# Performance work log

Hardware: AMD Instinct MI355X
Metric: run time of the kernel (lower is better)

Reference implementation:

```python
import jax, jax.numpy as jnp
import numpy as np

N_HEAD = 12

def setup_inputs() -> dict:
    key = jax.random.key(0)
    k1, k2, k3 = jax.random.split(key, 3)
    nx = 768
    B, S = 2, 2048
    return {
        "hidden_states": jax.random.normal(k1, (B, S, nx), dtype=jnp.float32),
        "w_attn": jax.random.normal(k2, (nx, 3 * nx), dtype=jnp.float32) * 0.02,
        "b_attn": jnp.zeros((3 * nx,), dtype=jnp.float32),
        "w_proj": jax.random.normal(k3, (nx, nx), dtype=jnp.float32) * 0.02,
        "b_proj": jnp.zeros((nx,), dtype=jnp.float32),
    }

def reference(hidden_states, w_attn, b_attn, w_proj, b_proj):
    B, S, nx = hidden_states.shape
    d_head = nx // N_HEAD
    qkv = hidden_states @ w_attn + b_attn  # [B,S,3nx]
    q, k, v = jnp.split(qkv, 3, axis=-1)
    # split heads -> [B,H,S,d]
    def split(x):
        return x.reshape(B, S, N_HEAD, d_head).transpose(0, 2, 1, 3)
    q, k, v = split(q), split(k), split(v)
    # scale=True: divide by sqrt(d_head) (v.size(-1))
    w = jnp.einsum("bhsd,bhtd->bhst", q, k) / jnp.sqrt(jnp.float32(d_head))
    w = jax.nn.softmax(w, axis=-1)
    a = jnp.einsum("bhst,bhtd->bhsd", w, v)  # [B,H,S,d]
    a = a.transpose(0, 2, 1, 3).reshape(B, S, nx)  # merge heads
    return a @ w_proj + b_proj
```

## Files before the change

kernel.cpp:

```cpp
#include <hip/hip_runtime.h>

#define NHEAD 12
#define DHEAD 64
#define SEQ   2048
#define NB    2
#define NX    768
#define MTOK  (NB * SEQ)

typedef __attribute__((ext_vector_type(8))) short short8;
typedef __attribute__((ext_vector_type(4))) short short4v;
typedef __attribute__((ext_vector_type(4))) float f32x4;

__device__ __forceinline__ unsigned short f2bf(float x) {
    union { float f; unsigned u; } v; v.f = x;
    unsigned r = v.u + 0x7fffu + ((v.u >> 16) & 1u);
    return (unsigned short)(r >> 16);
}

#define MFMA32(a, b, c) __builtin_amdgcn_mfma_f32_16x16x32_bf16(a, b, c, 0, 0, 0)
#define MFMA16(a, b, c) __builtin_amdgcn_mfma_f32_16x16x16bf16_1k(a, b, c, 0, 0, 0)

__global__ __launch_bounds__(256)
void cvt_all(const float* __restrict__ hs,
             const float* __restrict__ wa, const float* __restrict__ wp,
             unsigned short* __restrict__ Abf,
             unsigned short* __restrict__ WtA, unsigned short* __restrict__ WtP)
{
    __shared__ float tile[32][33];
    const int bid = blockIdx.x;
    const int t = threadIdx.x;

    if (bid < 3072) {
        int i = bid * 256 + t;
        if (i >= 786432) return;
        float4 v = ((const float4*)hs)[i];
        ushort4 o;
        o.x = f2bf(v.x); o.y = f2bf(v.y); o.z = f2bf(v.z); o.w = f2bf(v.w);
        ((ushort4*)Abf)[i] = o;
        return;
    }

    const float* W; unsigned short* T; int K, N, bx, by;
    if (bid < 4800) {
        int b2 = bid - 3072;
        bx = b2 % 72; by = b2 / 72;
        W = wa; T = WtA; K = NX; N = 3 * NX;
    } else {
        int b2 = bid - 4800;
        bx = b2 % 24; by = b2 / 24;
        W = wp; T = WtP; K = NX; N = NX;
    }
    const int r = t >> 5, c = t & 31;
    const int k0 = by * 32, n0 = bx * 32;
#pragma unroll
    for (int i = 0; i < 4; i++)
        tile[r + i * 8][c] = W[(size_t)(k0 + r + i * 8) * N + n0 + c];
    __syncthreads();
#pragma unroll
    for (int i = 0; i < 4; i++) {
        int n = r + i * 8;
        T[(size_t)(n0 + n) * K + k0 + c] = f2bf(tile[c][n]);
    }
}

template<int MODE>
__global__ __launch_bounds__(256, 3)
void gemm_bf(const unsigned short* __restrict__ A,
             const unsigned short* __restrict__ Bt,
             const float* __restrict__ bias,
             float* __restrict__ fo,
             unsigned short* __restrict__ qb, unsigned short* __restrict__ kb2,
             unsigned short* __restrict__ vtb,
             int M, int N, int K)
{
    __shared__ __align__(16) unsigned char sm[2][16384];
    const int t = threadIdx.x;
    const int w = t >> 6, lane = t & 63;
    const int lo16 = lane & 15, quad = lane >> 4;
    const int ib = blockIdx.y * 128, jb = blockIdx.x * 128;

    f32x4 acc[4][4];
#pragma unroll
    for (int mt = 0; mt < 4; mt++)
#pragma unroll
        for (int nt = 0; nt < 4; nt++) acc[mt][nt] = (f32x4){0.f, 0.f, 0.f, 0.f};

    const int srow = lane >> 2;
    const int sj   = lane & 3;

    auto stage = [&](int buf, int k0) {
#pragma unroll
        for (int i = 0; i < 4; i++) {
            const int u   = i * 4 + w;
            const int p   = u >> 3;
            const int row = (u & 7) * 16 + srow;
            const int sc  = sj ^ (row & 3);
            const unsigned short* g = (p == 0)
                ? (A  + (size_t)(ib + row) * K + k0 + sc * 8)
                : (Bt + (size_t)(jb + row) * K + k0 + sc * 8);
            void* lp = &sm[buf][p * 8192 + (u & 7) * 1024];
            __builtin_amdgcn_global_load_lds(
                (const __attribute__((address_space(1))) unsigned int*)g,
                (__attribute__((address_space(3))) unsigned int*)lp, 16, 0, 0);
        }
    };

    const int mrow = (w >> 1) * 64;
    const int nrow = (w & 1) * 64;

    stage(0, 0);
    const int NIT = K / 32;
    for (int kt = 0; kt < NIT; kt++) {
        const int buf = kt & 1;
        __syncthreads();
        if (kt + 1 < NIT) stage(buf ^ 1, (kt + 1) * 32);

        short8 af[4], bf[4];
#pragma unroll
        for (int mt = 0; mt < 4; mt++) {
            const int row = mrow + mt * 16 + lo16;
            af[mt] = *(const short8*)&sm[buf][row * 64 + ((quad ^ (row & 3)) * 16)];
        }
#pragma unroll
        for (int nt = 0; nt < 4; nt++) {
            const int row = nrow + nt * 16 + lo16;
            bf[nt] = *(const short8*)&sm[buf][8192 + row * 64 + ((quad ^ (row & 3)) * 16)];
        }
#pragma unroll
        for (int mt = 0; mt < 4; mt++)
#pragma unroll
            for (int nt = 0; nt < 4; nt++)
                acc[mt][nt] = MFMA32(af[mt], bf[nt], acc[mt][nt]);
    }

    if constexpr (MODE == 0) {
        const int which = jb / NX;
#pragma unroll
        for (int nt = 0; nt < 4; nt++) {
            const int j  = jb + nrow + nt * 16 + lo16;
            const int cc = j - which * NX;
            const int hh = cc >> 6, dd = cc & 63;
            const float bj = bias[j];
#pragma unroll
            for (int mt = 0; mt < 4; mt++) {
                const int m0 = ib + mrow + mt * 16 + quad * 4;
                const int bb = m0 >> 11;
                const int s0 = m0 & 2047;
                const size_t hb = (size_t)(bb * NHEAD + hh);
                if (which == 2) {
                    ushort4 pv;
                    pv.x = f2bf(acc[mt][nt][0] + bj);
                    pv.y = f2bf(acc[mt][nt][1] + bj);
                    pv.z = f2bf(acc[mt][nt][2] + bj);
                    pv.w = f2bf(acc[mt][nt][3] + bj);
                    *(ushort4*)(vtb + (hb * DHEAD + dd) * SEQ + s0) = pv;
                } else {
                    unsigned short* dst = (which == 0) ? qb : kb2;
                    const float sc = (which == 0) ? 0.125f : 1.0f;
#pragma unroll
                    for (int r = 0; r < 4; r++)
                        dst[(hb * SEQ + s0 + r) * DHEAD + dd] =
                            f2bf((acc[mt][nt][r] + bj) * sc);
                }
            }
        }
    } else {
#pragma unroll
        for (int nt = 0; nt < 4; nt++) {
            const int j  = jb + nrow + nt * 16 + lo16;
            const float bj = bias[j];
#pragma unroll
            for (int mt = 0; mt < 4; mt++) {
                const int m0 = ib + mrow + mt * 16 + quad * 4;
#pragma unroll
                for (int r = 0; r < 4; r++)
                    fo[(size_t)(m0 + r) * N + j] = acc[mt][nt][r] + bj;
            }
        }
    }
}

__global__ __launch_bounds__(256, 3)
void attn_bf(const unsigned short* __restrict__ qb, const unsigned short* __restrict__ kb,
             const unsigned short* __restrict__ vtb, unsigned short* __restrict__ ab)
{
    __shared__ __align__(16) unsigned char sm[2][16384];
    const int t = threadIdx.x;
    const int w = t >> 6, lane = t & 63;
    const int lo16 = lane & 15, quad = lane >> 4;

    const int id = blockIdx.x;
    const int xcd = id & 7, slot = id >> 3;
    const int bh = xcd * 3 + slot % 3;
    const int q0 = (slot / 3) * 64;
    const int b = bh / NHEAD, h = bh % NHEAD;

    const unsigned short* Qb = qb  + (size_t)bh * SEQ * DHEAD;
    const unsigned short* Kb = kb  + (size_t)bh * SEQ * DHEAD;
    const unsigned short* Vb = vtb + (size_t)bh * DHEAD * SEQ;

    short8 qf[2];
    {
        const size_t qo = (size_t)(q0 + w * 16 + lo16) * DHEAD + quad * 8;
        qf[0] = *(const short8*)(Qb + qo);
        qf[1] = *(const short8*)(Qb + qo + 32);
    }

    const int srow = lane >> 3;
    const int sj   = lane & 7;
    auto stage = [&](int buf, int k0) {
#pragma unroll
        for (int i = 0; i < 4; i++) {
            const int u   = i * 4 + w;
            const int p   = u >> 3;
            const int row = (u & 7) * 8 + srow;
            const int sc  = sj ^ (row & 7);
            const unsigned short* g = (p == 0)
                ? (Kb + (size_t)(k0 + row) * DHEAD + sc * 8)
                : (Vb + (size_t)row * SEQ + k0 + sc * 8);
            void* lp = &sm[buf][p * 8192 + (u & 7) * 1024];
            __builtin_amdgcn_global_load_lds(
                (const __attribute__((address_space(1))) unsigned int*)g,
                (__attribute__((address_space(3))) unsigned int*)lp, 16, 0, 0);
        }
    };

    f32x4 oacc[4];
#pragma unroll
    for (int dt = 0; dt < 4; dt++) oacc[dt] = (f32x4){0.f, 0.f, 0.f, 0.f};
    float lsum = 0.f;

    stage(0, 0);
    for (int kt = 0; kt < SEQ / 64; kt++) {
        const int buf = kt & 1;
        __syncthreads();
        if (kt + 1 < SEQ / 64) stage(buf ^ 1, (kt + 1) * 64);

        f32x4 s[4];
#pragma unroll
        for (int rt = 0; rt < 4; rt++) {
            const int row = rt * 16 + lo16;
            const int rs = row & 7;
            short8 kf0 = *(const short8*)&sm[buf][row * 128 + ((quad ^ rs) * 16)];
            short8 kf1 = *(const short8*)&sm[buf][row * 128 + (((4 + quad) ^ rs) * 16)];
            f32x4 a = (f32x4){0.f, 0.f, 0.f, 0.f};
            a = MFMA32(kf0, qf[0], a);
            a = MFMA32(kf1, qf[1], a);
            s[rt] = a;
        }

        short4v pf[4];
#pragma unroll
        for (int rt = 0; rt < 4; rt++) {
            float p0 = __expf(s[rt][0]), p1 = __expf(s[rt][1]);
            float p2 = __expf(s[rt][2]), p3 = __expf(s[rt][3]);
            lsum += (p0 + p1) + (p2 + p3);
            short4v pv;
            pv[0] = (short)f2bf(p0); pv[1] = (short)f2bf(p1);
            pv[2] = (short)f2bf(p2); pv[3] = (short)f2bf(p3);
            pf[rt] = pv;
        }

#pragma unroll
        for (int dt = 0; dt < 4; dt++) {
            const int row = dt * 16 + lo16;
            const int rs = row & 7;
            f32x4 a = oacc[dt];
#pragma unroll
            for (int rt = 0; rt < 4; rt++) {
                const int ch = (2 * rt + (quad >> 1)) ^ rs;
                short4v vf = *(const short4v*)&sm[buf][8192 + row * 128 + ch * 16 + (quad & 1) * 8];
                a = MFMA16(vf, pf[rt], a);
            }
            oacc[dt] = a;
        }
    }

    lsum += __shfl_xor(lsum, 16);
    lsum += __shfl_xor(lsum, 32);
    const float inv = 1.0f / lsum;

    unsigned short* dst = ab + (size_t)(b * SEQ + q0 + w * 16 + lo16) * NX + h * DHEAD;
#pragma unroll
    for (int dt = 0; dt < 4; dt++) {
        ushort4 pv;
        pv.x = f2bf(oacc[dt][0] * inv);
        pv.y = f2bf(oacc[dt][1] * inv);
        pv.z = f2bf(oacc[dt][2] * inv);
        pv.w = f2bf(oacc[dt][3] * inv);
        *(ushort4*)(dst + dt * 16 + quad * 4) = pv;
    }
}

extern "C" void kernel_launch(void* const* d_in, const int* in_sizes, int n_in,
                              void* d_out, int out_size, void* d_ws, size_t ws_size,
                              hipStream_t stream)
{
    const float* hs     = (const float*)d_in[0];
    const float* w_attn = (const float*)d_in[1];
    const float* b_attn = (const float*)d_in[2];
    const float* w_proj = (const float*)d_in[3];
    const float* b_proj = (const float*)d_in[4];
    float* out = (float*)d_out;

    unsigned short* wsu = (unsigned short*)d_ws;
    unsigned short* Abf  = wsu;
    unsigned short* WtA  = Abf  + 3145728;
    unsigned short* WtP  = WtA  + 1769472;
    unsigned short* qbuf = WtP  + 589824;
    unsigned short* kbuf = qbuf + 3145728;
    unsigned short* vtbf = kbuf + 3145728;
    unsigned short* abf  = vtbf + 3145728;

    cvt_all<<<5376, 256, 0, stream>>>(hs, w_attn, w_proj, Abf, WtA, WtP);

    gemm_bf<0><<<dim3(18, 32), 256, 0, stream>>>(
        Abf, WtA, b_attn, nullptr, qbuf, kbuf, vtbf, MTOK, 3 * NX, NX);

    attn_bf<<<768, 256, 0, stream>>>(qbuf, kbuf, vtbf, abf);

    gemm_bf<1><<<dim3(6, 32), 256, 0, stream>>>(
        abf, WtP, b_proj, out, nullptr, nullptr, nullptr, MTOK, NX, NX);
}
```

Measured before the change: 162.7 us.

## Split QKV GEMM into transposed Q/K and V launches, widen attention query tiles

The QKV GEMM is split into two launches. Q/K are computed with swapped operands so each lane writes contiguous ushort4 along the head dimension, and V keeps the transposed layout. The output projection is likewise swapped so it writes float4 rows. The attention kernel moves to 128 threads with two query tiles per wave, so each staged K/V tile feeds twice the MFMA work. Q is prescaled by log2(e)/sqrt(d) so exp2 can be used, and bf16 packing uses a byte-permute truncation instead of round-to-nearest, which costs a little precision and raises register pressure per wave.

```diff
diff --git a/kernel.cpp b/kernel.cpp
--- a/kernel.cpp
+++ b/kernel.cpp
@@ -19,6 +19,8 @@
 
 #define MFMA32(a, b, c) __builtin_amdgcn_mfma_f32_16x16x32_bf16(a, b, c, 0, 0, 0)
 #define MFMA16(a, b, c) __builtin_amdgcn_mfma_f32_16x16x16bf16_1k(a, b, c, 0, 0, 0)
+
+#define QSCALE 0.1803368801111204f
 
 __global__ __launch_bounds__(256)
 void cvt_all(const float* __restrict__ hs,
@@ -134,12 +136,10 @@
     }
 
     if constexpr (MODE == 0) {
-        const int which = jb / NX;
 #pragma unroll
         for (int nt = 0; nt < 4; nt++) {
             const int j  = jb + nrow + nt * 16 + lo16;
-            const int cc = j - which * NX;
-            const int hh = cc >> 6, dd = cc & 63;
+            const int hh = j >> 6, dd = j & 63;
             const float bj = bias[j];
 #pragma unroll
             for (int mt = 0; mt < 4; mt++) {
@@ -147,40 +147,58 @@
                 const int bb = m0 >> 11;
                 const int s0 = m0 & 2047;
                 const size_t hb = (size_t)(bb * NHEAD + hh);
-                if (which == 2) {
-                    ushort4 pv;
-                    pv.x = f2bf(acc[mt][nt][0] + bj);
-                    pv.y = f2bf(acc[mt][nt][1] + bj);
-                    pv.z = f2bf(acc[mt][nt][2] + bj);
-                    pv.w = f2bf(acc[mt][nt][3] + bj);
-                    *(ushort4*)(vtb + (hb * DHEAD + dd) * SEQ + s0) = pv;
-                } else {
-                    unsigned short* dst = (which == 0) ? qb : kb2;
-                    const float sc = (which == 0) ? 0.125f : 1.0f;
-#pragma unroll
-                    for (int r = 0; r < 4; r++)
-                        dst[(hb * SEQ + s0 + r) * DHEAD + dd] =
-                            f2bf((acc[mt][nt][r] + bj) * sc);
-                }
+                ushort4 pv;
+                pv.x = f2bf(acc[mt][nt][0] + bj);
+                pv.y = f2bf(acc[mt][nt][1] + bj);
+                pv.z = f2bf(acc[mt][nt][2] + bj);
+                pv.w = f2bf(acc[mt][nt][3] + bj);
+                *(ushort4*)(vtb + (hb * DHEAD + dd) * SEQ + s0) = pv;
+            }
+        }
+    } else if constexpr (MODE == 2) {
+#pragma unroll
+        for (int mt = 0; mt < 4; mt++) {
+            const int ch0   = ib + mrow + mt * 16 + quad * 4;
+            const int which = ch0 / NX;
+            const int cc    = ch0 - which * NX;
+            const int hh    = cc >> 6, dd = cc & 63;
+            const float4 bv = *(const float4*)(bias + ch0);
+            unsigned short* dst = which ? kb2 : qb;
+            const float sc = which ? 1.0f : QSCALE;
+#pragma unroll
+            for (int nt = 0; nt < 4; nt++) {
+                const int tok = jb + nrow + nt * 16 + lo16;
+                const int bb  = tok >> 11;
+                const int s0  = tok & 2047;
+                const size_t hb = (size_t)(bb * NHEAD + hh);
+                ushort4 pv;
+                pv.x = f2bf((acc[mt][nt][0] + bv.x) * sc);
+                pv.y = f2bf((acc[mt][nt][1] + bv.y) * sc);
+                pv.z = f2bf((acc[mt][nt][2] + bv.z) * sc);
+                pv.w = f2bf((acc[mt][nt][3] + bv.w) * sc);
+                *(ushort4*)(dst + (hb * SEQ + s0) * DHEAD + dd) = pv;
             }
         }
     } else {
 #pragma unroll
-        for (int nt = 0; nt < 4; nt++) {
-            const int j  = jb + nrow + nt * 16 + lo16;
-            const float bj = bias[j];
-#pragma unroll
-            for (int mt = 0; mt < 4; mt++) {
-                const int m0 = ib + mrow + mt * 16 + quad * 4;
-#pragma unroll
-                for (int r = 0; r < 4; r++)
-                    fo[(size_t)(m0 + r) * N + j] = acc[mt][nt][r] + bj;
-            }
-        }
-    }
-}
-
-__global__ __launch_bounds__(256, 3)
+        for (int mt = 0; mt < 4; mt++) {
+            const int ch0   = ib + mrow + mt * 16 + quad * 4;
+            const float4 bv = *(const float4*)(bias + ch0);
+#pragma unroll
+            for (int nt = 0; nt < 4; nt++) {
+                const int tok = jb + nrow + nt * 16 + lo16;
+                float4 v;
+                v.x = acc[mt][nt][0] + bv.x;
+                v.y = acc[mt][nt][1] + bv.y;
+                v.z = acc[mt][nt][2] + bv.z;
+                v.w = acc[mt][nt][3] + bv.w;
+                *(float4*)(fo + (size_t)tok * NX + ch0) = v;
+            }
+        }
+    }
+}
+
+__global__ __launch_bounds__(128, 2)
 void attn_bf(const unsigned short* __restrict__ qb, const unsigned short* __restrict__ kb,
              const unsigned short* __restrict__ vtb, unsigned short* __restrict__ ab)
 {
@@ -199,19 +217,20 @@
     const unsigned short* Kb = kb  + (size_t)bh * SEQ * DHEAD;
     const unsigned short* Vb = vtb + (size_t)bh * DHEAD * SEQ;
 
-    short8 qf[2];
-    {
-        const size_t qo = (size_t)(q0 + w * 16 + lo16) * DHEAD + quad * 8;
-        qf[0] = *(const short8*)(Qb + qo);
-        qf[1] = *(const short8*)(Qb + qo + 32);
+    short8 qf[2][2];
+#pragma unroll
+    for (int qt = 0; qt < 2; qt++) {
+        const size_t qo = (size_t)(q0 + w * 32 + qt * 16 + lo16) * DHEAD + quad * 8;
+        qf[qt][0] = *(const short8*)(Qb + qo);
+        qf[qt][1] = *(const short8*)(Qb + qo + 32);
     }
 
     const int srow = lane >> 3;
     const int sj   = lane & 7;
     auto stage = [&](int buf, int k0) {
 #pragma unroll
-        for (int i = 0; i < 4; i++) {
-            const int u   = i * 4 + w;
+        for (int i = 0; i < 8; i++) {
+            const int u   = i * 2 + w;
             const int p   = u >> 3;
             const int row = (u & 7) * 8 + srow;
             const int sc  = sj ^ (row & 7);
@@ -225,10 +244,14 @@
         }
     };
 
-    f32x4 oacc[4];
-#pragma unroll
-    for (int dt = 0; dt < 4; dt++) oacc[dt] = (f32x4){0.f, 0.f, 0.f, 0.f};
-    float lsum = 0.f;
+    f32x4 oacc[4][2];
+#pragma unroll
+    for (int dt = 0; dt < 4; dt++)
+#pragma unroll
+        for (int qt = 0; qt < 2; qt++) oacc[dt][qt] = (f32x4){0.f, 0.f, 0.f, 0.f};
+    float lsum[2] = {0.f, 0.f};
+
+    const unsigned sel = 0x07060302u;
 
     stage(0, 0);
     for (int kt = 0; kt < SEQ / 64; kt++) {
@@ -236,59 +259,73 @@
         __syncthreads();
         if (kt + 1 < SEQ / 64) stage(buf ^ 1, (kt + 1) * 64);
 
-        f32x4 s[4];
+        f32x4 s[4][2];
 #pragma unroll
         for (int rt = 0; rt < 4; rt++) {
             const int row = rt * 16 + lo16;
             const int rs = row & 7;
             short8 kf0 = *(const short8*)&sm[buf][row * 128 + ((quad ^ rs) * 16)];
             short8 kf1 = *(const short8*)&sm[buf][row * 128 + (((4 + quad) ^ rs) * 16)];
-            f32x4 a = (f32x4){0.f, 0.f, 0.f, 0.f};
-            a = MFMA32(kf0, qf[0], a);
-            a = MFMA32(kf1, qf[1], a);
-            s[rt] = a;
-        }
-
-        short4v pf[4];
-#pragma unroll
-        for (int rt = 0; rt < 4; rt++) {
-            float p0 = __expf(s[rt][0]), p1 = __expf(s[rt][1]);
-            float p2 = __expf(s[rt][2]), p3 = __expf(s[rt][3]);
-            lsum += (p0 + p1) + (p2 + p3);
-            short4v pv;
-            pv[0] = (short)f2bf(p0); pv[1] = (short)f2bf(p1);
-            pv[2] = (short)f2bf(p2); pv[3] = (short)f2bf(p3);
-            pf[rt] = pv;
-        }
+#pragma unroll
+            for (int qt = 0; qt < 2; qt++) {
+                f32x4 a = (f32x4){0.f, 0.f, 0.f, 0.f};
+                a = MFMA32(kf0, qf[qt][0], a);
+                a = MFMA32(kf1, qf[qt][1], a);
+                s[rt][qt] = a;
+            }
+        }
+
+        short4v pf[4][2];
+#pragma unroll
+        for (int rt = 0; rt < 4; rt++)
+#pragma unroll
+            for (int qt = 0; qt < 2; qt++) {
+                union { float f; unsigned u; } p0, p1, p2, p3;
+                p0.f = __builtin_amdgcn_exp2f(s[rt][qt][0]);
+                p1.f = __builtin_amdgcn_exp2f(s[rt][qt][1]);
+                p2.f = __builtin_amdgcn_exp2f(s[rt][qt][2]);
+                p3.f = __builtin_amdgcn_exp2f(s[rt][qt][3]);
+                lsum[qt] += (p0.f + p1.f) + (p2.f + p3.f);
+                union { unsigned u[2]; short4v v; } pk;
+                pk.u[0] = __builtin_amdgcn_perm(p1.u, p0.u, sel);
+                pk.u[1] = __builtin_amdgcn_perm(p3.u, p2.u, sel);
+                pf[rt][qt] = pk.v;
+            }
 
 #pragma unroll
         for (int dt = 0; dt < 4; dt++) {
             const int row = dt * 16 + lo16;
             const int rs = row & 7;
-            f32x4 a = oacc[dt];
 #pragma unroll
             for (int rt = 0; rt < 4; rt++) {
                 const int ch = (2 * rt + (quad >> 1)) ^ rs;
                 short4v vf = *(const short4v*)&sm[buf][8192 + row * 128 + ch * 16 + (quad & 1) * 8];
-                a = MFMA16(vf, pf[rt], a);
-            }
-            oacc[dt] = a;
-        }
-    }
-
-    lsum += __shfl_xor(lsum, 16);
-    lsum += __shfl_xor(lsum, 32);
-    const float inv = 1.0f / lsum;
-
-    unsigned short* dst = ab + (size_t)(b * SEQ + q0 + w * 16 + lo16) * NX + h * DHEAD;
-#pragma unroll
-    for (int dt = 0; dt < 4; dt++) {
-        ushort4 pv;
-        pv.x = f2bf(oacc[dt][0] * inv);
-        pv.y = f2bf(oacc[dt][1] * inv);
-        pv.z = f2bf(oacc[dt][2] * inv);
-        pv.w = f2bf(oacc[dt][3] * inv);
-        *(ushort4*)(dst + dt * 16 + quad * 4) = pv;
+#pragma unroll
+                for (int qt = 0; qt < 2; qt++)
+                    oacc[dt][qt] = MFMA16(vf, pf[rt][qt], oacc[dt][qt]);
+            }
+        }
+    }
+
+#pragma unroll
+    for (int qt = 0; qt < 2; qt++) {
+        lsum[qt] += __shfl_xor(lsum[qt], 16);
+        lsum[qt] += __shfl_xor(lsum[qt], 32);
+    }
+
+#pragma unroll
+    for (int qt = 0; qt < 2; qt++) {
+        const float inv = 1.0f / lsum[qt];
+        unsigned short* dst = ab + (size_t)(b * SEQ + q0 + w * 32 + qt * 16 + lo16) * NX + h * DHEAD;
+#pragma unroll
+        for (int dt = 0; dt < 4; dt++) {
+            ushort4 pv;
+            pv.x = f2bf(oacc[dt][qt][0] * inv);
+            pv.y = f2bf(oacc[dt][qt][1] * inv);
+            pv.z = f2bf(oacc[dt][qt][2] * inv);
+            pv.w = f2bf(oacc[dt][qt][3] * inv);
+            *(ushort4*)(dst + dt * 16 + quad * 4) = pv;
+        }
     }
 }
 
@@ -314,11 +351,15 @@
 
     cvt_all<<<5376, 256, 0, stream>>>(hs, w_attn, w_proj, Abf, WtA, WtP);
 
-    gemm_bf<0><<<dim3(18, 32), 256, 0, stream>>>(
-        Abf, WtA, b_attn, nullptr, qbuf, kbuf, vtbf, MTOK, 3 * NX, NX);
-
-    attn_bf<<<768, 256, 0, stream>>>(qbuf, kbuf, vtbf, abf);
-
-    gemm_bf<1><<<dim3(6, 32), 256, 0, stream>>>(
-        abf, WtP, b_proj, out, nullptr, nullptr, nullptr, MTOK, NX, NX);
-}
+    gemm_bf<2><<<dim3(32, 12), 256, 0, stream>>>(
+        WtA, Abf, b_attn, nullptr, qbuf, kbuf, nullptr, 1536, MTOK, NX);
+
+    gemm_bf<0><<<dim3(6, 32), 256, 0, stream>>>(
+        Abf, WtA + 1536 * NX, b_attn + 1536, nullptr, nullptr, nullptr, vtbf,
+        MTOK, NX, NX);
+
+    attn_bf<<<768, 128, 0, stream>>>(qbuf, kbuf, vtbf, abf);
+
+    gemm_bf<3><<<dim3(32, 6), 256, 0, stream>>>(
+        WtP, abf, b_proj, out, nullptr, nullptr, nullptr, NX, MTOK, NX);
+}
```

New measurement: 176.0 us. +8.2%, slower.
